# Kernel tuning notes

Hardware: AMD Instinct MI355X
Metric: run time of the kernel (lower is better)

The kernel has to match this reference:

```python
import jax, jax.numpy as jnp
import numpy as np

STRIDE, K, PAD = 2, 4, 1
DN = ('NCH', 'OIH', 'NCH')


def conv1d(x, w, b):
    # w: (out, in, k); stride-2, pad-1 conv matching nn.Conv1d(k=4,s=2,p=1)
    y = jax.lax.conv_general_dilated(x, w, (STRIDE,), ((PAD, PAD),), dimension_numbers=DN)
    return y + b[None, :, None]


def conv_transpose1d(x, w, b):
    # w: (in, out, k) torch ConvTranspose1d layout. Equivalent forward conv:
    # dilate input by stride, pad k-1-p=2 each side, flipped+transposed kernel.
    wf = jnp.flip(w, -1).transpose(1, 0, 2)  # (out, in, k)
    y = jax.lax.conv_general_dilated(x, wf, (1,), ((K - 1 - PAD, K - 1 - PAD),),
                                     lhs_dilation=(STRIDE,), dimension_numbers=DN)
    return y + b[None, :, None]


def setup_inputs() -> dict:
    key = jax.random.key(0)
    ks = jax.random.split(key, 9)
    s = 0.1  # keep activations stable through 6 layers
    return {
        'x': jax.random.normal(ks[0], (16, 1, 65536), dtype=jnp.float32),
        'enc_w0': jax.random.normal(ks[1], (64, 1, 4), dtype=jnp.float32) * s,
        'enc_w': jax.random.normal(ks[2], (5, 64, 64, 4), dtype=jnp.float32) * s,
        'enc_b': jax.random.normal(ks[3], (6, 64), dtype=jnp.float32) * s,
        'codebook': jax.random.normal(ks[4], (1024, 64), dtype=jnp.float32),
        'dec_w': jax.random.normal(ks[5], (5, 64, 64, 4), dtype=jnp.float32) * s,
        'dec_w_last': jax.random.normal(ks[6], (64, 1, 4), dtype=jnp.float32) * s,
        'dec_b': jax.random.normal(ks[7], (5, 64), dtype=jnp.float32) * s,
        'dec_b_last': jax.random.normal(ks[8], (1,), dtype=jnp.float32) * s,
    }


def reference(x, enc_w0, enc_w, enc_b, codebook, dec_w, dec_w_last, dec_b, dec_b_last):
    B = x.shape[0]
    D = codebook.shape[1]

    h = jax.nn.relu(conv1d(x, enc_w0, enc_b[0]))
    for i in range(5):
        h = jax.nn.relu(conv1d(h, enc_w[i], enc_b[i + 1]))
    # h: (B, D, L'); flatten tokens
    z_e = h.transpose(0, 2, 1).reshape(-1, D)  # (B*L', D)

    # ---- Vector quantize: squared-distance argmin + gather ----
    dist = (jnp.sum(z_e * z_e, axis=1, keepdims=True)
            - 2.0 * z_e @ codebook.T
            + jnp.sum(codebook * codebook, axis=1)[None, :])  # (B*L', C)
    ids = jnp.argmin(dist, axis=-1)
    e = codebook[ids]
    e_k = z_e + jax.lax.stop_gradient(e - z_e)  # straight-through

    g = e_k.reshape(B, -1, D).transpose(0, 2, 1)  # (B, D, L')

    for i in range(5):
        g = jax.nn.relu(conv_transpose1d(g, dec_w[i], dec_b[i]))
    y = conv_transpose1d(g, dec_w_last, dec_b_last)
    return y, z_e, ids
```

## Files before the change

### kernel.cpp

```cpp
#include <hip/hip_runtime.h>

#define CH 64
#define TILE 128

typedef short s16x8 __attribute__((ext_vector_type(8)));
typedef float f32x4 __attribute__((ext_vector_type(4)));

static __device__ __forceinline__ ushort f2bf(float f) {
    union { float f; uint u; } v; v.f = f;
    const uint r = (v.u + 0x7FFFu + ((v.u >> 16) & 1u)) >> 16;
    return (ushort)r;
}
static __device__ __forceinline__ float bf2f(ushort u) {
    union { uint u; float f; } v; v.u = ((uint)u) << 16; return v.f;
}

__global__ __launch_bounds__(256) void k_prepack_enc(
    const float* __restrict__ enc_w, float* __restrict__ encW)
{
    const int idx = blockIdx.x * 256 + threadIdx.x;
    const int tau = idx & 3;
    const int o = (idx >> 2) & 63;
    const int i = (idx >> 8) & 63;
    const int L = idx >> 14;
    encW[idx] = enc_w[(((size_t)L * 64 + o) * 64 + i) * 4 + tau];
}

__device__ __forceinline__ void stage_q(
    const float* __restrict__ inb, float (*inT)[264], int q,
    int m0, int Lin, int tid)
{
    const int r = tid >> 4;
    const int i = q * 16 + r;
    const int seg = tid & 15;
    const float* src = inb + (size_t)i * Lin + 2 * m0 + 16 * seg;
    float* dst = inT[r] + 1 + 16 * seg;
#pragma unroll
    for (int t = 0; t < 4; ++t) {
        const float4 v = *(const float4*)(src + 4 * t);
        float* d = dst + 4 * t;
        d[0] = v.x;
        *(float2*)(d + 1) = make_float2(v.y, v.z);
        d[3] = v.w;
    }
    if (tid < 32) {
        const int rr = tid & 15, side = tid >> 4;
        const int pl = side ? 257 : 0;
        const int p = 2 * m0 - 1 + pl;
        inT[rr][pl] = (p >= 0 && p < Lin) ? inb[(size_t)(q * 16 + rr) * Lin + p] : 0.f;
    }
}

__device__ __forceinline__ void conv_accum_q(
    const float (*inT)[264], const float* __restrict__ wpk, int ibase,
    float acc[4][8], int og, int pg)
{
    const float* wI = wpk + og * 16 + (size_t)ibase * 256;
    for (int ii = 0; ii < 16; ++ii) {
        const float* wp = wI + ii * 256;
        const float4 w0 = *(const float4*)(wp + 0);
        const float4 w1 = *(const float4*)(wp + 4);
        const float4 w2 = *(const float4*)(wp + 8);
        const float4 w3 = *(const float4*)(wp + 12);
        const float* row = inT[ii];
#pragma unroll
        for (int j = 0; j < 4; ++j) {
            const int base = 4 * pg + 64 * j;
            const float2 xa = *(const float2*)(row + base);
            const float2 xb = *(const float2*)(row + base + 2);
            const float2 xc = *(const float2*)(row + base + 4);
            acc[0][2*j]   += w0.x * xa.x + w0.y * xa.y + w0.z * xb.x + w0.w * xb.y;
            acc[1][2*j]   += w1.x * xa.x + w1.y * xa.y + w1.z * xb.x + w1.w * xb.y;
            acc[2][2*j]   += w2.x * xa.x + w2.y * xa.y + w2.z * xb.x + w2.w * xb.y;
            acc[3][2*j]   += w3.x * xa.x + w3.y * xa.y + w3.z * xb.x + w3.w * xb.y;
            acc[0][2*j+1] += w0.x * xb.x + w0.y * xb.y + w0.z * xc.x + w0.w * xc.y;
            acc[1][2*j+1] += w1.x * xb.x + w1.y * xb.y + w1.z * xc.x + w1.w * xc.y;
            acc[2][2*j+1] += w2.x * xb.x + w2.y * xb.y + w2.z * xc.x + w2.w * xc.y;
            acc[3][2*j+1] += w3.x * xb.x + w3.y * xb.y + w3.z * xc.x + w3.w * xc.y;
        }
    }
}

__device__ __forceinline__ void conv_epilogue(
    float acc[4][8], float* __restrict__ out,
    int b, int m0, int Lout, int transpose, int og, int pg)
{
    if (!transpose) {
#pragma unroll
        for (int oo = 0; oo < 4; ++oo) {
            float* ob = out + ((size_t)b * CH + og * 4 + oo) * Lout + m0 + 2 * pg;
#pragma unroll
            for (int j = 0; j < 4; ++j) {
                float2 v;
                v.x = fmaxf(acc[oo][2*j], 0.f);
                v.y = fmaxf(acc[oo][2*j+1], 0.f);
                *(float2*)(ob + 32 * j) = v;
            }
        }
    } else {
#pragma unroll
        for (int j = 0; j < 4; ++j)
#pragma unroll
            for (int h = 0; h < 2; ++h) {
                const int ml = 2 * pg + 32 * j + h;
                float* ob = out + ((size_t)b * Lout + m0 + ml) * CH + og * 4;
                float4 v;
                v.x = fmaxf(acc[0][2*j+h], 0.f);
                v.y = fmaxf(acc[1][2*j+h], 0.f);
                v.z = fmaxf(acc[2][2*j+h], 0.f);
                v.w = fmaxf(acc[3][2*j+h], 0.f);
                *(float4*)ob = v;
            }
    }
}

__global__ __launch_bounds__(256) void k_enc_conv(
    const float* __restrict__ in, const float* __restrict__ wpk,
    const float* __restrict__ bias, float* __restrict__ out,
    int Lin, int Lout, int transpose)
{
    __shared__ float inT[16][264];
    const int m0 = blockIdx.x * TILE;
    const int b = blockIdx.y;
    const int tid = threadIdx.x;
    const int og = tid >> 4, pg = tid & 15;
    const float* inb = in + (size_t)b * CH * Lin;
    float acc[4][8];
#pragma unroll
    for (int oo = 0; oo < 4; ++oo) {
        const float bv = bias[og * 4 + oo];
#pragma unroll
        for (int j = 0; j < 8; ++j) acc[oo][j] = bv;
    }
    for (int q = 0; q < 4; ++q) {
        stage_q(inb, inT, q, m0, Lin, tid);
        __syncthreads();
        conv_accum_q(inT, wpk, q * 16, acc, og, pg);
        __syncthreads();
    }
    conv_epilogue(acc, out, b, m0, Lout, transpose, og, pg);
}

__global__ __launch_bounds__(256) void k_enc01(
    const float* __restrict__ x, const float* __restrict__ w0,
    const float* __restrict__ b0, const float* __restrict__ wpk0,
    const float* __restrict__ b1, float* __restrict__ out)
{
    __shared__ float xl[520];
    __shared__ float e0s[16][264];
    const int m0 = blockIdx.x * TILE;
    const int b = blockIdx.y;
    const int tid = threadIdx.x;
    const int og = tid >> 4, pg = tid & 15;
    const float* xb = x + (size_t)b * 65536;
    const int x0i = 4 * m0 - 3;
    for (int xi = tid; xi < 518; xi += 256) {
        const int q = x0i + xi;
        xl[xi] = (q >= 0 && q < 65536) ? xb[q] : 0.f;
    }
    float acc[4][8];
#pragma unroll
    for (int oo = 0; oo < 4; ++oo) {
        const float bv = b1[og * 4 + oo];
#pragma unroll
        for (int j = 0; j < 8; ++j) acc[oo][j] = bv;
    }
    const int r = tid >> 4;
    const int oct = tid & 15;
    const int pbase = 2 * m0 - 1;
    __syncthreads();
    for (int q = 0; q < 4; ++q) {
        {
            const int i = q * 16 + r;
            const float4 wv = *(const float4*)(w0 + i * 4);
            const float bv = b0[i];
            for (int t = 0; t < 17; ++t) {
                const int pl = oct * 17 + t;
                if (pl < 258) {
                    const int pe = pbase + pl;
                    const float* xp = xl + 2 * pl;
                    const float v = wv.x * xp[0] + wv.y * xp[1] + wv.z * xp[2] + wv.w * xp[3] + bv;
                    e0s[r][pl] = (pe >= 0 && pe < 32768) ? fmaxf(v, 0.f) : 0.f;
                }
            }
        }
        __syncthreads();
        conv_accum_q(e0s, wpk0, q * 16, acc, og, pg);
        __syncthreads();
    }
    conv_epilogue(acc, out, b, m0, 16384, 0, og, pg);
}

__global__ __launch_bounds__(512) void k_vq(
    const float* __restrict__ z, const float* __restrict__ cb,
    float* __restrict__ idsf, ushort* __restrict__ g)
{
    __shared__ float c2s[1024];
    __shared__ float rval[8][64];
    __shared__ int   ridx[8][64];
    __shared__ int   widx[64];
    const int t0 = blockIdx.x * 64;
    const int tid = threadIdx.x;
    const int lane = tid & 63;
    const int wv = __builtin_amdgcn_readfirstlane(tid >> 6);

    for (int c = tid; c < 1024; c += 512) {
        const float* cp = cb + (size_t)c * 64;
        float s0 = 0.f, s1 = 0.f, s2 = 0.f, s3 = 0.f;
#pragma unroll
        for (int d = 0; d < 64; d += 4) {
            const float4 v = *(const float4*)(cp + d);
            s0 += v.x * v.x; s1 += v.y * v.y; s2 += v.z * v.z; s3 += v.w * v.w;
        }
        c2s[c] = (s0 + s1) + (s2 + s3);
    }
    float pz[64];
    {
        const float* zp = z + (size_t)(t0 + lane) * 64;
#pragma unroll
        for (int d = 0; d < 64; d += 4) {
            const float4 v = *(const float4*)(zp + d);
            pz[d] = -2.f * v.x; pz[d + 1] = -2.f * v.y;
            pz[d + 2] = -2.f * v.z; pz[d + 3] = -2.f * v.w;
        }
    }
    __syncthreads();
    float best = 3.0e38f; int bidx = 0;
    const int cbase = wv * 128;
    for (int cc = 0; cc < 128; ++cc) {
        const int code = cbase + cc;
        const float* cp = cb + (size_t)code * 64;
        float a0 = 0.f, a1 = 0.f, a2 = 0.f, a3 = 0.f;
#pragma unroll
        for (int d = 0; d < 64; d += 4) {
            a0 += cp[d] * pz[d];
            a1 += cp[d + 1] * pz[d + 1];
            a2 += cp[d + 2] * pz[d + 2];
            a3 += cp[d + 3] * pz[d + 3];
        }
        const float dist = c2s[code] + ((a0 + a1) + (a2 + a3));
        if (dist < best) { best = dist; bidx = code; }
    }
    rval[wv][lane] = best; ridx[wv][lane] = bidx;
    __syncthreads();
    if (tid < 64) {
        float bv = rval[0][tid]; int bi = ridx[0][tid];
#pragma unroll
        for (int k2 = 1; k2 < 8; ++k2) {
            const float v = rval[k2][tid];
            if (v < bv) { bv = v; bi = ridx[k2][tid]; }
        }
        widx[tid] = bi;
        idsf[t0 + tid] = (float)bi;
    }
    __syncthreads();
    const int bb = t0 >> 10;
    const int mb = t0 & 1023;
    ushort* gb = g + ((size_t)bb * 1026 + 1 + mb) * 64;
    for (int e = tid; e < 4096; e += 512) {
        const int d = e & 63;
        const int tok = e >> 6;
        gb[(size_t)tok * 64 + d] = f2bf(cb[(size_t)widx[tok] * 64 + d]);
    }
    if (mb == 0 && tid < 16) {
        ushort4 zz = {0, 0, 0, 0};
        *(ushort4*)(g + ((size_t)bb * 1026) * 64 + tid * 4) = zz;
    }
    if (mb == 960 && tid < 16) {
        ushort4 zz = {0, 0, 0, 0};
        *(ushort4*)(g + ((size_t)bb * 1026 + 1025) * 64 + tid * 4) = zz;
    }
}

__global__ __launch_bounds__(256) void k_prepack(
    const float* __restrict__ dec_w, ushort* __restrict__ Afrag)
{
    const int idx = blockIdx.x * 256 + threadIdx.x;
    const int j    = idx & 7;
    const int lane = (idx >> 3) & 63;
    const int kt   = (idx >> 9) & 1;
    const int m    = (idx >> 10) & 3;
    const int tap  = (idx >> 12) & 3;
    const int L    = idx >> 14;
    const int o = m * 16 + (lane & 15);
    const int i = kt * 32 + ((lane >> 4) << 3) + j;
    Afrag[idx] = f2bf(dec_w[(((size_t)L * 64 + i) * 64 + o) * 4 + tap]);
}

__device__ __forceinline__ void dec_mfma_compute_g(
    const ushort* __restrict__ Xb, const ushort* __restrict__ AfragL,
    int u0, int tid, f32x4 accE[4], f32x4 accO[4],
    int& ul_out, int& kg_out)
{
    const int lane = tid & 63;
    const int wave = tid >> 6;
    const int col = lane & 15, kg = lane >> 4;
    const int ul = wave * 16 + col;
    const ushort* basep = Xb + (size_t)(u0 + ul) * 64 + kg * 8;
    s16x8 Bm1[2], B0[2], Bp1[2];
#pragma unroll
    for (int kt = 0; kt < 2; ++kt) {
        Bm1[kt] = *(const s16x8*)(basep - 64 + kt * 32);
        B0[kt]  = *(const s16x8*)(basep + kt * 32);
        Bp1[kt] = *(const s16x8*)(basep + 64 + kt * 32);
    }
    const s16x8* Af = (const s16x8*)AfragL;
#pragma unroll
    for (int m = 0; m < 4; ++m) {
        f32x4 aE = {0.f, 0.f, 0.f, 0.f};
        f32x4 aO = {0.f, 0.f, 0.f, 0.f};
#pragma unroll
        for (int kt = 0; kt < 2; ++kt) {
            aE = __builtin_amdgcn_mfma_f32_16x16x32_bf16(
                Af[((1 * 4 + m) * 2 + kt) * 64 + lane], B0[kt], aE, 0, 0, 0);
            aE = __builtin_amdgcn_mfma_f32_16x16x32_bf16(
                Af[((3 * 4 + m) * 2 + kt) * 64 + lane], Bm1[kt], aE, 0, 0, 0);
            aO = __builtin_amdgcn_mfma_f32_16x16x32_bf16(
                Af[((2 * 4 + m) * 2 + kt) * 64 + lane], B0[kt], aO, 0, 0, 0);
            aO = __builtin_amdgcn_mfma_f32_16x16x32_bf16(
                Af[((0 * 4 + m) * 2 + kt) * 64 + lane], Bp1[kt], aO, 0, 0, 0);
        }
        accE[m] = aE;
        accO[m] = aO;
    }
    ul_out = ul; kg_out = kg;
}

__global__ __launch_bounds__(64) void k_dec2(
    const ushort* __restrict__ Xt, const ushort* __restrict__ AfragL,
    const float* __restrict__ bias, ushort* __restrict__ Yt, int Lin)
{
    const int u0 = blockIdx.x * 16;
    const int b  = blockIdx.y;
    const int tid = threadIdx.x;
    const int Lout = Lin * 2;
    const ushort* Xb = Xt + ((size_t)b * (Lin + 2) + 1) * 64;
    ushort* Yb = Yt + ((size_t)b * (Lout + 2) + 1) * 64;

    f32x4 accE[4], accO[4];
    int ul, kg;
    dec_mfma_compute_g(Xb, AfragL, u0, tid, accE, accO, ul, kg);
    const size_t n2 = 2 * (size_t)(u0 + ul);
#pragma unroll
    for (int m = 0; m < 4; ++m) {
        const float4 bm4 = *(const float4*)(bias + m * 16 + kg * 4);
        const float bb[4] = {bm4.x, bm4.y, bm4.z, bm4.w};
        ushort4 pe, po;
        pe.x = f2bf(fmaxf(accE[m][0] + bb[0], 0.f));
        pe.y = f2bf(fmaxf(accE[m][1] + bb[1], 0.f));
        pe.z = f2bf(fmaxf(accE[m][2] + bb[2], 0.f));
        pe.w = f2bf(fmaxf(accE[m][3] + bb[3], 0.f));
        po.x = f2bf(fmaxf(accO[m][0] + bb[0], 0.f));
        po.y = f2bf(fmaxf(accO[m][1] + bb[1], 0.f));
        po.z = f2bf(fmaxf(accO[m][2] + bb[2], 0.f));
        po.w = f2bf(fmaxf(accO[m][3] + bb[3], 0.f));
        *(ushort4*)(Yb + n2 * 64 + m * 16 + kg * 4) = pe;
        *(ushort4*)(Yb + (n2 + 1) * 64 + m * 16 + kg * 4) = po;
    }
    if (blockIdx.x == 0 && tid < 16) {
        ushort4 zz = {0, 0, 0, 0};
        *(ushort4*)(Yt + ((size_t)b * (Lout + 2)) * 64 + tid * 4) = zz;
    }
    if (u0 + 16 >= Lin && tid < 16) {
        ushort4 zz = {0, 0, 0, 0};
        *(ushort4*)(Yb + (size_t)Lout * 64 + tid * 4) = zz;
    }
}

__global__ __launch_bounds__(256) void k_dec4y(
    const ushort* __restrict__ Xt, const ushort* __restrict__ AfragL,
    const float* __restrict__ w4, const float* __restrict__ bias,
    const float* __restrict__ wl, const float* __restrict__ blp,
    float* __restrict__ y)
{
    __shared__ float d4s[64][130];
    const int u0 = blockIdx.x * 64;
    const int b  = blockIdx.y;
    const int tid = threadIdx.x;
    const int Lin = 16384;
    const ushort* Xb = Xt + ((size_t)b * (Lin + 2) + 1) * 64;

    f32x4 accE[4], accO[4];
    int ul, kg;
    dec_mfma_compute_g(Xb, AfragL, u0, tid, accE, accO, ul, kg);
#pragma unroll
    for (int m = 0; m < 4; ++m) {
        const float4 bm4 = *(const float4*)(bias + m * 16 + kg * 4);
        const float bb[4] = {bm4.x, bm4.y, bm4.z, bm4.w};
#pragma unroll
        for (int r = 0; r < 4; ++r) {
            const int o = m * 16 + kg * 4 + r;
            d4s[o][2 * ul + 1] = fmaxf(accE[m][r] + bb[r], 0.f);
            d4s[o][2 * ul + 2] = fmaxf(accO[m][r] + bb[r], 0.f);
        }
    }
    {
        const int side = tid >> 7;
        const int o = (tid >> 1) & 63;
        const int half = tid & 1;
        const int ib = half * 32;
        float p0 = 0.f, p1 = 0.f;
        const ushort* r0 = Xb + (size_t)(side ? (u0 + 64) : (u0 - 1)) * 64;
        const ushort* r1 = Xb + (size_t)(side ? (u0 + 63) : u0) * 64;
        const int tA = side ? 1 : 2;
        const int tB = side ? 3 : 0;
        for (int i = ib; i < ib + 32; i += 2) {
            const float* wpa = w4 + ((size_t)i * 64 + o) * 4;
            const float* wpb = w4 + ((size_t)(i + 1) * 64 + o) * 4;
            p0 += wpa[tA] * bf2f(r0[i]) + wpa[tB] * bf2f(r1[i]);
            p1 += wpb[tA] * bf2f(r0[i + 1]) + wpb[tB] * bf2f(r1[i + 1]);
        }
        float part = p0 + p1;
        part += __shfl_xor(part, 1);
        if (half == 0) {
            const float acc = bias[o] + part;
            if (side == 0) d4s[o][0]   = (u0 > 0)          ? fmaxf(acc, 0.f) : 0.f;
            else           d4s[o][129] = (u0 + 64 < 16384) ? fmaxf(acc, 0.f) : 0.f;
        }
    }
    __syncthreads();
    {
        const int odd = tid & 1;
        const int vl = (tid >> 1) + 1;
        float a0 = 0.f, a1 = 0.f, a2 = 0.f, a3 = 0.f;
        for (int o = 0; o < 64; o += 4) {
            const float4 w0 = *(const float4*)(wl + (o + 0) * 4);
            const float4 w1 = *(const float4*)(wl + (o + 1) * 4);
            const float4 w2 = *(const float4*)(wl + (o + 2) * 4);
            const float4 w3 = *(const float4*)(wl + (o + 3) * 4);
            const float xv0 = d4s[o + 0][vl], xn0 = d4s[o + 0][odd ? vl + 1 : vl - 1];
            const float xv1 = d4s[o + 1][vl], xn1 = d4s[o + 1][odd ? vl + 1 : vl - 1];
            const float xv2 = d4s[o + 2][vl], xn2 = d4s[o + 2][odd ? vl + 1 : vl - 1];
            const float xv3 = d4s[o + 3][vl], xn3 = d4s[o + 3][odd ? vl + 1 : vl - 1];
            a0 += odd ? (w0.z * xv0 + w0.x * xn0) : (w0.y * xv0 + w0.w * xn0);
            a1 += odd ? (w1.z * xv1 + w1.x * xn1) : (w1.y * xv1 + w1.w * xn1);
            a2 += odd ? (w2.z * xv2 + w2.x * xn2) : (w2.y * xv2 + w2.w * xn2);
            a3 += odd ? (w3.z * xv3 + w3.x * xn3) : (w3.y * xv3 + w3.w * xn3);
        }
        y[(size_t)b * 65536 + 4 * u0 + tid] = blp[0] + ((a0 + a1) + (a2 + a3));
    }
}

extern "C" void kernel_launch(void* const* d_in, const int* in_sizes, int n_in,
                              void* d_out, int out_size, void* d_ws, size_t ws_size,
                              hipStream_t stream) {
    const float* x      = (const float*)d_in[0];
    const float* enc_w0 = (const float*)d_in[1];
    const float* enc_w  = (const float*)d_in[2];
    const float* enc_b  = (const float*)d_in[3];
    const float* cb     = (const float*)d_in[4];
    const float* dec_w  = (const float*)d_in[5];
    const float* dec_wl = (const float*)d_in[6];
    const float* dec_b  = (const float*)d_in[7];
    const float* dec_bl = (const float*)d_in[8];
    float* y    = (float*)d_out;
    float* z_e  = y + 1048576;
    float* idsf = y + 2097152;

    float* A  = (float*)d_ws;
    float* Bf = A + 16777216;

    float*  encW  = y + 14 * 65536;
    ushort* Afrag = (ushort*)(encW + 81920);

    k_prepack_enc<<<dim3(320), 256, 0, stream>>>(enc_w, encW);
    k_prepack<<<dim3(320), 256, 0, stream>>>(dec_w, Afrag);

    k_enc01<<<dim3(128, 16), 256, 0, stream>>>(x, enc_w0, enc_b, encW, enc_b + 64, A);
    k_enc_conv<<<dim3(64, 16), 256, 0, stream>>>(A,  encW + 1 * 16384, enc_b + 2 * 64, Bf, 16384, 8192, 0);
    k_enc_conv<<<dim3(32, 16), 256, 0, stream>>>(Bf, encW + 2 * 16384, enc_b + 3 * 64, A,  8192,  4096, 0);
    k_enc_conv<<<dim3(16, 16), 256, 0, stream>>>(A,  encW + 3 * 16384, enc_b + 4 * 64, Bf, 4096,  2048, 0);
    k_enc_conv<<<dim3(8, 16),  256, 0, stream>>>(Bf, encW + 4 * 16384, enc_b + 5 * 64, z_e, 2048, 1024, 1);
    k_vq<<<256, 512, 0, stream>>>(z_e, cb, idsf, (ushort*)A);

    k_dec2<<<dim3(64, 16),  64, 0, stream>>>((const ushort*)A,  Afrag + 0 * 16384, dec_b + 0 * 64, (ushort*)Bf, 1024);
    k_dec2<<<dim3(128, 16), 64, 0, stream>>>((const ushort*)Bf, Afrag + 1 * 16384, dec_b + 1 * 64, (ushort*)A,  2048);
    k_dec2<<<dim3(256, 16), 64, 0, stream>>>((const ushort*)A,  Afrag + 2 * 16384, dec_b + 2 * 64, (ushort*)Bf, 4096);
    k_dec2<<<dim3(512, 16), 64, 0, stream>>>((const ushort*)Bf, Afrag + 3 * 16384, dec_b + 3 * 64, (ushort*)A,  8192);
    (void)hipMemcpyAsync(Bf, Afrag + 4 * 16384, 16384 * sizeof(ushort),
                         hipMemcpyDeviceToDevice, stream);
    k_dec4y<<<dim3(256, 16), 256, 0, stream>>>((const ushort*)A, (const ushort*)Bf,
                                               dec_w + 4 * 16384, dec_b + 4 * 64,
                                               dec_wl, dec_bl, y);
}
```

Baseline: 523.2 us.

## Pack encoder conv accumulators as float2 and split decoder output channels across blocks

The encoder conv inner loop now keeps its accumulators as two-wide float vectors. Each vector pairs positions 64 apart, which lets the compiler emit packed FMA instructions, and the epilogue store addressing is updated to match. The small decoder kernels gain a third grid dimension that splits the four 16-channel output groups into two halves, doubling block count so the short early layers fill more compute units. The cost is that each decoder block reloads the same input fragments, and the helper function is inlined separately into the two kernels.

```diff
diff --git a/kernel.cpp b/kernel.cpp
--- a/kernel.cpp
+++ b/kernel.cpp
@@ -5,6 +5,7 @@
 
 typedef short s16x8 __attribute__((ext_vector_type(8)));
 typedef float f32x4 __attribute__((ext_vector_type(4)));
+typedef float f32x2 __attribute__((ext_vector_type(2)));
 
 static __device__ __forceinline__ ushort f2bf(float f) {
     union { float f; uint u; } v; v.f = f;
@@ -53,7 +54,7 @@
 
 __device__ __forceinline__ void conv_accum_q(
     const float (*inT)[264], const float* __restrict__ wpk, int ibase,
-    float acc[4][8], int og, int pg)
+    f32x2 acc2[4][4], int og, int pg)
 {
     const float* wI = wpk + og * 16 + (size_t)ibase * 256;
     for (int ii = 0; ii < 16; ++ii) {
@@ -64,25 +65,28 @@
         const float4 w3 = *(const float4*)(wp + 12);
         const float* row = inT[ii];
 #pragma unroll
-        for (int j = 0; j < 4; ++j) {
-            const int base = 4 * pg + 64 * j;
-            const float2 xa = *(const float2*)(row + base);
-            const float2 xb = *(const float2*)(row + base + 2);
-            const float2 xc = *(const float2*)(row + base + 4);
-            acc[0][2*j]   += w0.x * xa.x + w0.y * xa.y + w0.z * xb.x + w0.w * xb.y;
-            acc[1][2*j]   += w1.x * xa.x + w1.y * xa.y + w1.z * xb.x + w1.w * xb.y;
-            acc[2][2*j]   += w2.x * xa.x + w2.y * xa.y + w2.z * xb.x + w2.w * xb.y;
-            acc[3][2*j]   += w3.x * xa.x + w3.y * xa.y + w3.z * xb.x + w3.w * xb.y;
-            acc[0][2*j+1] += w0.x * xb.x + w0.y * xb.y + w0.z * xc.x + w0.w * xc.y;
-            acc[1][2*j+1] += w1.x * xb.x + w1.y * xb.y + w1.z * xc.x + w1.w * xc.y;
-            acc[2][2*j+1] += w2.x * xb.x + w2.y * xb.y + w2.z * xc.x + w2.w * xc.y;
-            acc[3][2*j+1] += w3.x * xb.x + w3.y * xb.y + w3.z * xc.x + w3.w * xc.y;
+        for (int jp = 0; jp < 2; ++jp) {
+            const float* rp = row + 4 * pg + 64 * jp;
+            const f32x2 t0 = {rp[0], rp[128]};
+            const f32x2 t1 = {rp[1], rp[129]};
+            const f32x2 t2 = {rp[2], rp[130]};
+            const f32x2 t3 = {rp[3], rp[131]};
+            const f32x2 t4 = {rp[4], rp[132]};
+            const f32x2 t5 = {rp[5], rp[133]};
+            acc2[0][2*jp]   += w0.x * t0 + w0.y * t1 + w0.z * t2 + w0.w * t3;
+            acc2[0][2*jp+1] += w0.x * t2 + w0.y * t3 + w0.z * t4 + w0.w * t5;
+            acc2[1][2*jp]   += w1.x * t0 + w1.y * t1 + w1.z * t2 + w1.w * t3;
+            acc2[1][2*jp+1] += w1.x * t2 + w1.y * t3 + w1.z * t4 + w1.w * t5;
+            acc2[2][2*jp]   += w2.x * t0 + w2.y * t1 + w2.z * t2 + w2.w * t3;
+            acc2[2][2*jp+1] += w2.x * t2 + w2.y * t3 + w2.z * t4 + w2.w * t5;
+            acc2[3][2*jp]   += w3.x * t0 + w3.y * t1 + w3.z * t2 + w3.w * t3;
+            acc2[3][2*jp+1] += w3.x * t2 + w3.y * t3 + w3.z * t4 + w3.w * t5;
         }
     }
 }
 
 __device__ __forceinline__ void conv_epilogue(
-    float acc[4][8], float* __restrict__ out,
+    f32x2 acc2[4][4], float* __restrict__ out,
     int b, int m0, int Lout, int transpose, int og, int pg)
 {
     if (!transpose) {
@@ -90,26 +94,35 @@
         for (int oo = 0; oo < 4; ++oo) {
             float* ob = out + ((size_t)b * CH + og * 4 + oo) * Lout + m0 + 2 * pg;
 #pragma unroll
-            for (int j = 0; j < 4; ++j) {
-                float2 v;
-                v.x = fmaxf(acc[oo][2*j], 0.f);
-                v.y = fmaxf(acc[oo][2*j+1], 0.f);
-                *(float2*)(ob + 32 * j) = v;
+            for (int jp = 0; jp < 2; ++jp) {
+                float2 vlo, vhi;
+                vlo.x = fmaxf(acc2[oo][2*jp].x, 0.f);
+                vlo.y = fmaxf(acc2[oo][2*jp+1].x, 0.f);
+                vhi.x = fmaxf(acc2[oo][2*jp].y, 0.f);
+                vhi.y = fmaxf(acc2[oo][2*jp+1].y, 0.f);
+                *(float2*)(ob + 32 * jp) = vlo;
+                *(float2*)(ob + 32 * jp + 64) = vhi;
             }
         }
     } else {
 #pragma unroll
-        for (int j = 0; j < 4; ++j)
+        for (int jp = 0; jp < 2; ++jp)
 #pragma unroll
             for (int h = 0; h < 2; ++h) {
-                const int ml = 2 * pg + 32 * j + h;
-                float* ob = out + ((size_t)b * Lout + m0 + ml) * CH + og * 4;
-                float4 v;
-                v.x = fmaxf(acc[0][2*j+h], 0.f);
-                v.y = fmaxf(acc[1][2*j+h], 0.f);
-                v.z = fmaxf(acc[2][2*j+h], 0.f);
-                v.w = fmaxf(acc[3][2*j+h], 0.f);
-                *(float4*)ob = v;
+                const int ml = 2 * pg + 32 * jp + h;
+                float* ob0 = out + ((size_t)b * Lout + m0 + ml) * CH + og * 4;
+                float* ob1 = out + ((size_t)b * Lout + m0 + ml + 64) * CH + og * 4;
+                float4 v0, v1;
+                v0.x = fmaxf(acc2[0][2*jp+h].x, 0.f);
+                v0.y = fmaxf(acc2[1][2*jp+h].x, 0.f);
+                v0.z = fmaxf(acc2[2][2*jp+h].x, 0.f);
+                v0.w = fmaxf(acc2[3][2*jp+h].x, 0.f);
+                v1.x = fmaxf(acc2[0][2*jp+h].y, 0.f);
+                v1.y = fmaxf(acc2[1][2*jp+h].y, 0.f);
+                v1.z = fmaxf(acc2[2][2*jp+h].y, 0.f);
+                v1.w = fmaxf(acc2[3][2*jp+h].y, 0.f);
+                *(float4*)ob0 = v0;
+                *(float4*)ob1 = v1;
             }
     }
 }
@@ -125,20 +138,20 @@
     const int tid = threadIdx.x;
     const int og = tid >> 4, pg = tid & 15;
     const float* inb = in + (size_t)b * CH * Lin;
-    float acc[4][8];
+    f32x2 acc2[4][4];
 #pragma unroll
     for (int oo = 0; oo < 4; ++oo) {
         const float bv = bias[og * 4 + oo];
 #pragma unroll
-        for (int j = 0; j < 8; ++j) acc[oo][j] = bv;
+        for (int s = 0; s < 4; ++s) acc2[oo][s] = bv;
     }
     for (int q = 0; q < 4; ++q) {
         stage_q(inb, inT, q, m0, Lin, tid);
         __syncthreads();
-        conv_accum_q(inT, wpk, q * 16, acc, og, pg);
+        conv_accum_q(inT, wpk, q * 16, acc2, og, pg);
         __syncthreads();
     }
-    conv_epilogue(acc, out, b, m0, Lout, transpose, og, pg);
+    conv_epilogue(acc2, out, b, m0, Lout, transpose, og, pg);
 }
 
 __global__ __launch_bounds__(256) void k_enc01(
@@ -158,12 +171,12 @@
         const int q = x0i + xi;
         xl[xi] = (q >= 0 && q < 65536) ? xb[q] : 0.f;
     }
-    float acc[4][8];
+    f32x2 acc2[4][4];
 #pragma unroll
     for (int oo = 0; oo < 4; ++oo) {
         const float bv = b1[og * 4 + oo];
 #pragma unroll
-        for (int j = 0; j < 8; ++j) acc[oo][j] = bv;
+        for (int s = 0; s < 4; ++s) acc2[oo][s] = bv;
     }
     const int r = tid >> 4;
     const int oct = tid & 15;
@@ -185,10 +198,10 @@
             }
         }
         __syncthreads();
-        conv_accum_q(e0s, wpk0, q * 16, acc, og, pg);
+        conv_accum_q(e0s, wpk0, q * 16, acc2, og, pg);
         __syncthreads();
     }
-    conv_epilogue(acc, out, b, m0, 16384, 0, og, pg);
+    conv_epilogue(acc2, out, b, m0, 16384, 0, og, pg);
 }
 
 __global__ __launch_bounds__(512) void k_vq(
@@ -287,15 +300,21 @@
     Afrag[idx] = f2bf(dec_w[(((size_t)L * 64 + i) * 64 + o) * 4 + tap]);
 }
 
-__device__ __forceinline__ void dec_mfma_compute_g(
-    const ushort* __restrict__ Xb, const ushort* __restrict__ AfragL,
-    int u0, int tid, f32x4 accE[4], f32x4 accO[4],
-    int& ul_out, int& kg_out)
-{
+__global__ __launch_bounds__(64) void k_dec2(
+    const ushort* __restrict__ Xt, const ushort* __restrict__ AfragL,
+    const float* __restrict__ bias, ushort* __restrict__ Yt, int Lin)
+{
+    const int u0 = blockIdx.x * 16;
+    const int b  = blockIdx.y;
+    const int mb2 = blockIdx.z * 2;
+    const int tid = threadIdx.x;
+    const int Lout = Lin * 2;
+    const ushort* Xb = Xt + ((size_t)b * (Lin + 2) + 1) * 64;
+    ushort* Yb = Yt + ((size_t)b * (Lout + 2) + 1) * 64;
+
     const int lane = tid & 63;
-    const int wave = tid >> 6;
     const int col = lane & 15, kg = lane >> 4;
-    const int ul = wave * 16 + col;
+    const int ul = col;
     const ushort* basep = Xb + (size_t)(u0 + ul) * 64 + kg * 8;
     s16x8 Bm1[2], B0[2], Bp1[2];
 #pragma unroll
@@ -305,8 +324,10 @@
         Bp1[kt] = *(const s16x8*)(basep + 64 + kt * 32);
     }
     const s16x8* Af = (const s16x8*)AfragL;
-#pragma unroll
-    for (int m = 0; m < 4; ++m) {
+    const size_t n2 = 2 * (size_t)(u0 + ul);
+#pragma unroll
+    for (int mi = 0; mi < 2; ++mi) {
+        const int m = mb2 + mi;
         f32x4 aE = {0.f, 0.f, 0.f, 0.f};
         f32x4 aO = {0.f, 0.f, 0.f, 0.f};
 #pragma unroll
@@ -320,50 +341,29 @@
             aO = __builtin_amdgcn_mfma_f32_16x16x32_bf16(
                 Af[((0 * 4 + m) * 2 + kt) * 64 + lane], Bp1[kt], aO, 0, 0, 0);
         }
-        accE[m] = aE;
-        accO[m] = aO;
-    }
-    ul_out = ul; kg_out = kg;
-}
-
-__global__ __launch_bounds__(64) void k_dec2(
-    const ushort* __restrict__ Xt, const ushort* __restrict__ AfragL,
-    const float* __restrict__ bias, ushort* __restrict__ Yt, int Lin)
-{
-    const int u0 = blockIdx.x * 16;
-    const int b  = blockIdx.y;
-    const int tid = threadIdx.x;
-    const int Lout = Lin * 2;
-    const ushort* Xb = Xt + ((size_t)b * (Lin + 2) + 1) * 64;
-    ushort* Yb = Yt + ((size_t)b * (Lout + 2) + 1) * 64;
-
-    f32x4 accE[4], accO[4];
-    int ul, kg;
-    dec_mfma_compute_g(Xb, AfragL, u0, tid, accE, accO, ul, kg);
-    const size_t n2 = 2 * (size_t)(u0 + ul);
-#pragma unroll
-    for (int m = 0; m < 4; ++m) {
         const float4 bm4 = *(const float4*)(bias + m * 16 + kg * 4);
         const float bb[4] = {bm4.x, bm4.y, bm4.z, bm4.w};
         ushort4 pe, po;
-        pe.x = f2bf(fmaxf(accE[m][0] + bb[0], 0.f));
-        pe.y = f2bf(fmaxf(accE[m][1] + bb[1], 0.f));
-        pe.z = f2bf(fmaxf(accE[m][2] + bb[2], 0.f));
-        pe.w = f2bf(fmaxf(accE[m][3] + bb[3], 0.f));
-        po.x = f2bf(fmaxf(accO[m][0] + bb[0], 0.f));
-        po.y = f2bf(fmaxf(accO[m][1] + bb[1], 0.f));
-        po.z = f2bf(fmaxf(accO[m][2] + bb[2], 0.f));
-        po.w = f2bf(fmaxf(accO[m][3] + bb[3], 0.f));
+        pe.x = f2bf(fmaxf(aE[0] + bb[0], 0.f));
+        pe.y = f2bf(fmaxf(aE[1] + bb[1], 0.f));
+        pe.z = f2bf(fmaxf(aE[2] + bb[2], 0.f));
+        pe.w = f2bf(fmaxf(aE[3] + bb[3], 0.f));
+        po.x = f2bf(fmaxf(aO[0] + bb[0], 0.f));
+        po.y = f2bf(fmaxf(aO[1] + bb[1], 0.f));
+        po.z = f2bf(fmaxf(aO[2] + bb[2], 0.f));
+        po.w = f2bf(fmaxf(aO[3] + bb[3], 0.f));
         *(ushort4*)(Yb + n2 * 64 + m * 16 + kg * 4) = pe;
         *(ushort4*)(Yb + (n2 + 1) * 64 + m * 16 + kg * 4) = po;
     }
-    if (blockIdx.x == 0 && tid < 16) {
-        ushort4 zz = {0, 0, 0, 0};
-        *(ushort4*)(Yt + ((size_t)b * (Lout + 2)) * 64 + tid * 4) = zz;
-    }
-    if (u0 + 16 >= Lin && tid < 16) {
-        ushort4 zz = {0, 0, 0, 0};
-        *(ushort4*)(Yb + (size_t)Lout * 64 + tid * 4) = zz;
+    if (blockIdx.z == 0) {
+        if (blockIdx.x == 0 && tid < 16) {
+            ushort4 zz = {0, 0, 0, 0};
+            *(ushort4*)(Yt + ((size_t)b * (Lout + 2)) * 64 + tid * 4) = zz;
+        }
+        if (u0 + 16 >= Lin && tid < 16) {
+            ushort4 zz = {0, 0, 0, 0};
+            *(ushort4*)(Yb + (size_t)Lout * 64 + tid * 4) = zz;
+        }
     }
 }
 
@@ -380,18 +380,41 @@
     const int Lin = 16384;
     const ushort* Xb = Xt + ((size_t)b * (Lin + 2) + 1) * 64;
 
-    f32x4 accE[4], accO[4];
-    int ul, kg;
-    dec_mfma_compute_g(Xb, AfragL, u0, tid, accE, accO, ul, kg);
+    const int lane = tid & 63;
+    const int wave = tid >> 6;
+    const int col = lane & 15, kg = lane >> 4;
+    const int ul = wave * 16 + col;
+    const ushort* basep = Xb + (size_t)(u0 + ul) * 64 + kg * 8;
+    s16x8 Bm1[2], B0[2], Bp1[2];
+#pragma unroll
+    for (int kt = 0; kt < 2; ++kt) {
+        Bm1[kt] = *(const s16x8*)(basep - 64 + kt * 32);
+        B0[kt]  = *(const s16x8*)(basep + kt * 32);
+        Bp1[kt] = *(const s16x8*)(basep + 64 + kt * 32);
+    }
+    const s16x8* Af = (const s16x8*)AfragL;
 #pragma unroll
     for (int m = 0; m < 4; ++m) {
+        f32x4 aE = {0.f, 0.f, 0.f, 0.f};
+        f32x4 aO = {0.f, 0.f, 0.f, 0.f};
+#pragma unroll
+        for (int kt = 0; kt < 2; ++kt) {
+            aE = __builtin_amdgcn_mfma_f32_16x16x32_bf16(
+                Af[((1 * 4 + m) * 2 + kt) * 64 + lane], B0[kt], aE, 0, 0, 0);
+            aE = __builtin_amdgcn_mfma_f32_16x16x32_bf16(
+                Af[((3 * 4 + m) * 2 + kt) * 64 + lane], Bm1[kt], aE, 0, 0, 0);
+            aO = __builtin_amdgcn_mfma_f32_16x16x32_bf16(
+                Af[((2 * 4 + m) * 2 + kt) * 64 + lane], B0[kt], aO, 0, 0, 0);
+            aO = __builtin_amdgcn_mfma_f32_16x16x32_bf16(
+                Af[((0 * 4 + m) * 2 + kt) * 64 + lane], Bp1[kt], aO, 0, 0, 0);
+        }
         const float4 bm4 = *(const float4*)(bias + m * 16 + kg * 4);
         const float bb[4] = {bm4.x, bm4.y, bm4.z, bm4.w};
 #pragma unroll
         for (int r = 0; r < 4; ++r) {
             const int o = m * 16 + kg * 4 + r;
-            d4s[o][2 * ul + 1] = fmaxf(accE[m][r] + bb[r], 0.f);
-            d4s[o][2 * ul + 2] = fmaxf(accO[m][r] + bb[r], 0.f);
+            d4s[o][2 * ul + 1] = fmaxf(aE[r] + bb[r], 0.f);
+            d4s[o][2 * ul + 2] = fmaxf(aO[r] + bb[r], 0.f);
         }
     }
     {
@@ -473,10 +496,10 @@
     k_enc_conv<<<dim3(8, 16),  256, 0, stream>>>(Bf, encW + 4 * 16384, enc_b + 5 * 64, z_e, 2048, 1024, 1);
     k_vq<<<256, 512, 0, stream>>>(z_e, cb, idsf, (ushort*)A);
 
-    k_dec2<<<dim3(64, 16),  64, 0, stream>>>((const ushort*)A,  Afrag + 0 * 16384, dec_b + 0 * 64, (ushort*)Bf, 1024);
-    k_dec2<<<dim3(128, 16), 64, 0, stream>>>((const ushort*)Bf, Afrag + 1 * 16384, dec_b + 1 * 64, (ushort*)A,  2048);
-    k_dec2<<<dim3(256, 16), 64, 0, stream>>>((const ushort*)A,  Afrag + 2 * 16384, dec_b + 2 * 64, (ushort*)Bf, 4096);
-    k_dec2<<<dim3(512, 16), 64, 0, stream>>>((const ushort*)Bf, Afrag + 3 * 16384, dec_b + 3 * 64, (ushort*)A,  8192);
+    k_dec2<<<dim3(64, 16, 2),  64, 0, stream>>>((const ushort*)A,  Afrag + 0 * 16384, dec_b + 0 * 64, (ushort*)Bf, 1024);
+    k_dec2<<<dim3(128, 16, 2), 64, 0, stream>>>((const ushort*)Bf, Afrag + 1 * 16384, dec_b + 1 * 64, (ushort*)A,  2048);
+    k_dec2<<<dim3(256, 16, 2), 64, 0, stream>>>((const ushort*)A,  Afrag + 2 * 16384, dec_b + 2 * 64, (ushort*)Bf, 4096);
+    k_dec2<<<dim3(512, 16, 2), 64, 0, stream>>>((const ushort*)Bf, Afrag + 3 * 16384, dec_b + 3 * 64, (ushort*)A,  8192);
     (void)hipMemcpyAsync(Bf, Afrag + 4 * 16384, 16384 * sizeof(ushort),
                          hipMemcpyDeviceToDevice, stream);
     k_dec4y<<<dim3(256, 16), 256, 0, stream>>>((const ushort*)A, (const ushort*)Bf,
```

After: 573.2 us. 1.1x slower.
